# Kernel tuning notes

Hardware: AMD Instinct MI355X
Metric: run time of the kernel (lower is better)

Reference implementation:

```python
import jax, jax.numpy as jnp
import numpy as np

N = 50000   # nodes
E = 800000  # edges (avg degree 16)
D = 96      # feature dim (in = hidden = out)


def setup_inputs() -> dict:
    key = jax.random.key(0)
    ks = jax.random.split(key, 6)
    scale = 1.0 / np.sqrt(D)
    return {
        "x": jax.random.normal(ks[0], (N, D), jnp.float32),
        "edge_index": jax.random.randint(ks[1], (2, E), 0, N, dtype=jnp.int64),
        "W1": jax.random.normal(ks[2], (D, D), jnp.float32) * scale,
        "b1": jnp.zeros((D,), jnp.float32),
        "a1": jnp.full((1,), 0.25, jnp.float32),  # PReLU weight
        "W2": jax.random.normal(ks[3], (D, D), jnp.float32) * scale,
        "b2": jnp.zeros((D,), jnp.float32),
    }


def _gcn_conv(x, W, b, src, dst, norm, n):
    # GCNConv: linear transform, then degree-normalized scatter-add aggregation
    h = x @ W                               # [N, D_out]
    msg = h[src] * norm[:, None]            # gather + scale, [E+N, D_out]
    out = jax.ops.segment_sum(msg, dst, num_segments=n)
    return out + b


def reference(x, edge_index, W1, b1, a1, W2, b2):
    n = x.shape[0]
    # add self loops (PyG gcn_norm default, fill_value=1.0)
    loop = jnp.arange(n, dtype=edge_index.dtype)
    src = jnp.concatenate([edge_index[0], loop])
    dst = jnp.concatenate([edge_index[1], loop])
    # symmetric normalization: D^{-1/2} A D^{-1/2}
    ones = jnp.ones(src.shape[0], dtype=x.dtype)
    deg = jax.ops.segment_sum(ones, dst, num_segments=n)
    dinv = jnp.where(deg > 0, jax.lax.rsqrt(deg), 0.0)
    norm = dinv[src] * dinv[dst]

    h = _gcn_conv(x, W1, b1, src, dst, norm, n)
    h = jnp.where(h > 0, h, a1 * h)  # PReLU (dropout p=0.0 is a no-op)
    h = _gcn_conv(h, W2, b2, src, dst, norm, n)
    return h
```

## Files before the change

### kernel.cpp

```cpp
#include <hip/hip_runtime.h>
#include <hip/hip_bf16.h>

#define NNODES 50000
#define NEDGES 800000
#define DIM    96
#define NBUCK  196
#define CAP    4608
#define TM     64
#define XPAD   104
#define PCH    3125
#define NCHK   256
#define HP     256

typedef __attribute__((ext_vector_type(8))) short   short8;
typedef __attribute__((ext_vector_type(4))) float   float4v;

__device__ __forceinline__ float loadF(const void* p, long i, int isbf) {
    return isbf ? __bfloat162float(((const __hip_bfloat16*)p)[i])
                : ((const float*)p)[i];
}
__device__ __forceinline__ int clampN(int v) {
    return v < 0 ? 0 : (v >= NNODES ? NNODES - 1 : v);
}

__global__ void k_sniff(const unsigned* __restrict__ xw,
                        const unsigned* __restrict__ ew,
                        int* __restrict__ flags) {
    int lane = threadIdx.x;
    int bad = 0, nz = 0;
    for (int r = 0; r < 4; ++r) {
        unsigned w  = xw[lane + 64 * r];
        unsigned lo = w & 0xffffu;
        unsigned ex = (lo >> 7) & 0xffu;
        if (!(lo == 0u || (ex >= 90u && ex <= 145u))) bad++;
        unsigned o = ew[2 * (lane + 64 * r) + 1];
        if (o != 0u) nz++;
    }
    for (int off = 32; off; off >>= 1) {
        bad += __shfl_down(bad, off);
        nz  += __shfl_down(nz,  off);
    }
    if (lane == 0) {
        flags[0] = (bad <= 32) ? 1 : 0;
        flags[1] = (nz  <  4) ? 1 : 0;
    }
}

__global__ __launch_bounds__(256) void k_part(const int* __restrict__ w,
                                              const int* __restrict__ flags,
                                              int* __restrict__ hist,
                                              int* __restrict__ hoff,
                                              unsigned* __restrict__ ebuf) {
    __shared__ unsigned pack[PCH];
    __shared__ unsigned opack[PCH];
    __shared__ int h[256];
    __shared__ int sc[256];
    const int is64 = flags[1];
    const int tid = threadIdx.x;
    const int blk = blockIdx.x;
    const int e0  = blk * PCH;

    h[tid] = 0;
    __syncthreads();
    if (is64) {
        const long long* wl = (const long long*)w;
        for (int k = tid; k < PCH; k += 256) {
            int s = clampN((int)wl[e0 + k]);
            int d = clampN((int)wl[NEDGES + e0 + k]);
            pack[k] = ((unsigned)d << 16) | (unsigned)s;
            atomicAdd(&h[d >> 8], 1);
        }
    } else {
        for (int k = tid; k < PCH; k += 256) {
            int s = clampN(w[e0 + k]);
            int d = clampN(w[NEDGES + e0 + k]);
            pack[k] = ((unsigned)d << 16) | (unsigned)s;
            atomicAdd(&h[d >> 8], 1);
        }
    }
    __syncthreads();
    int v = h[tid];
    sc[tid] = v;
    __syncthreads();
    for (int off = 1; off < 256; off <<= 1) {
        int t2 = (tid >= off) ? sc[tid - off] : 0;
        __syncthreads();
        sc[tid] += t2;
        __syncthreads();
    }
    const int excl = sc[tid] - v;
    hist[blk * HP + tid] = v;
    hoff[blk * HP + tid] = excl;
    h[tid] = excl;
    __syncthreads();
    for (int k = tid; k < PCH; k += 256) {
        unsigned r = pack[k];
        int pos = atomicAdd(&h[(r >> 16) >> 8], 1);
        opack[pos] = r;
    }
    __syncthreads();
    for (int k = tid; k < PCH; k += 256)
        ebuf[e0 + k] = opack[k];
}

__global__ __launch_bounds__(512) void k_csr(const unsigned* __restrict__ ebuf,
                                             const int* __restrict__ hist,
                                             const int* __restrict__ hoff,
                                             int* __restrict__ rowbeg,
                                             int* __restrict__ rowend,
                                             unsigned short* __restrict__ col,
                                             float* __restrict__ dinv) {
    __shared__ int h256[256];
    __shared__ int sc[256];
    __shared__ int cur[256];
    __shared__ int scnt[256];
    __shared__ int soff[256];
    const int b   = blockIdx.x;
    const int tid = threadIdx.x;

    if (tid < 256) {
        scnt[tid] = hist[tid * HP + b];
        soff[tid] = hoff[tid * HP + b];
        h256[tid] = 0;
    }
    __syncthreads();
    const int ch  = tid >> 1;
    const int par = tid & 1;
    {
        const int cnt = scnt[ch];
        const int off = ch * PCH + soff[ch];
        for (int j = par; j < cnt; j += 2)
            atomicAdd(&h256[(ebuf[off + j] >> 16) & 255], 1);
    }
    __syncthreads();
    int v = 0;
    if (tid < 256) { v = h256[tid]; sc[tid] = v; }
    __syncthreads();
    for (int off = 1; off < 256; off <<= 1) {
        int t2 = 0;
        if (tid < 256 && tid >= off) t2 = sc[tid - off];
        __syncthreads();
        if (tid < 256) sc[tid] += t2;
        __syncthreads();
    }
    if (tid < 256) {
        int start = b * CAP + sc[tid] - v;
        cur[tid] = start;
        int node = b * 256 + tid;
        if (node < NNODES) {
            rowbeg[node] = start;
            rowend[node] = start + v;
            dinv[node] = rsqrtf((float)v + 1.0f);
        }
    }
    __syncthreads();
    {
        const int cnt = scnt[ch];
        const int off = ch * PCH + soff[ch];
        const int lim = (b + 1) * CAP;
        for (int j = par; j < cnt; j += 2) {
            unsigned r = ebuf[off + j];
            int pos = atomicAdd(&cur[(r >> 16) & 255], 1);
            if (pos < lim) col[pos] = (unsigned short)(r & 0xffffu);
        }
    }
}

__global__ __launch_bounds__(256) void k_gemm_mfma(
        const void* __restrict__ X, int x_force_bf16,
        const void* __restrict__ W,
        const float* __restrict__ dinv,
        __hip_bfloat16* __restrict__ g,
        const int* __restrict__ flags) {
    __shared__ __hip_bfloat16 Xs[TM * XPAD];
    __shared__ __hip_bfloat16 Wt[DIM * XPAD];

    const int t    = threadIdx.x;
    const int fbf  = flags[0];
    const int xbf  = x_force_bf16 ? 1 : fbf;
    const int row0 = blockIdx.x * TM;

    if (!fbf) {
        const float4* Wv = (const float4*)W;
        for (int idx = t; idx < DIM * DIM / 4; idx += 256) {
            int k = idx / (DIM / 4);
            int n = (idx - k * (DIM / 4)) * 4;
            float4 w4 = Wv[idx];
            Wt[(n + 0) * XPAD + k] = __float2bfloat16(w4.x);
            Wt[(n + 1) * XPAD + k] = __float2bfloat16(w4.y);
            Wt[(n + 2) * XPAD + k] = __float2bfloat16(w4.z);
            Wt[(n + 3) * XPAD + k] = __float2bfloat16(w4.w);
        }
    } else {
        for (int idx = t; idx < DIM * DIM; idx += 256) {
            int k = idx / DIM, n = idx - k * DIM;
            Wt[n * XPAD + k] = __float2bfloat16(loadF(W, idx, 1));
        }
    }
    if (!xbf) {
        const float4* Xv = (const float4*)X;
        for (int idx = t; idx < TM * (DIM / 4); idx += 256) {
            int r = idx / (DIM / 4);
            int c = (idx - r * (DIM / 4)) * 4;
            int gr = row0 + r;
            float4 vv = {0.f, 0.f, 0.f, 0.f};
            if (gr < NNODES) vv = Xv[(size_t)gr * (DIM / 4) + (c >> 2)];
            *(__hip_bfloat162*)&Xs[r * XPAD + c] =
                __halves2bfloat162(__float2bfloat16(vv.x), __float2bfloat16(vv.y));
            *(__hip_bfloat162*)&Xs[r * XPAD + c + 2] =
                __halves2bfloat162(__float2bfloat16(vv.z), __float2bfloat16(vv.w));
        }
    } else {
        const short* Xs16 = (const short*)X;
        for (int idx = t; idx < TM * (DIM / 8); idx += 256) {
            int r  = idx / (DIM / 8);
            int c8 = idx - r * (DIM / 8);
            int gr = row0 + r;
            short8 vv = {0, 0, 0, 0, 0, 0, 0, 0};
            if (gr < NNODES) vv = *(const short8*)(Xs16 + (size_t)gr * DIM + c8 * 8);
            *(short8*)((short*)Xs + r * XPAD + c8 * 8) = vv;
        }
    }
    __syncthreads();

    const int wave = t >> 6;
    const int lane = t & 63;
    const int m    = lane & 15;
    const int quad = lane >> 4;

    const short* xsp = (const short*)Xs;
    short8 a[3];
#pragma unroll
    for (int kt = 0; kt < 3; ++kt)
        a[kt] = *(const short8*)(xsp + (wave * 16 + m) * XPAD + kt * 32 + quad * 8);

    float dv[4];
#pragma unroll
    for (int r2 = 0; r2 < 4; ++r2) {
        int gr = row0 + wave * 16 + quad * 4 + r2;
        dv[r2] = (gr < NNODES) ? dinv[gr] : 0.f;
    }

    const short* wtp = (const short*)Wt;
#pragma unroll
    for (int nt = 0; nt < 6; ++nt) {
        float4v acc = {0.f, 0.f, 0.f, 0.f};
#pragma unroll
        for (int kt = 0; kt < 3; ++kt) {
            short8 b = *(const short8*)(wtp + (nt * 16 + m) * XPAD + kt * 32 + quad * 8);
            acc = __builtin_amdgcn_mfma_f32_16x16x32_bf16(a[kt], b, acc, 0, 0, 0);
        }
#pragma unroll
        for (int r2 = 0; r2 < 4; ++r2) {
            int gr = row0 + wave * 16 + quad * 4 + r2;
            if (gr < NNODES)
                g[(size_t)gr * DIM + nt * 16 + m] = __float2bfloat16(acc[r2] * dv[r2]);
        }
    }
}

__global__ __launch_bounds__(256) void k_aggr(
        const __hip_bfloat16* __restrict__ g,
        const int* __restrict__ rowbeg,
        const int* __restrict__ rowend,
        const unsigned short* __restrict__ col,
        const float* __restrict__ dinv,
        const void* __restrict__ b,
        const void* __restrict__ a1,
        void* __restrict__ out,
        const int* __restrict__ flags, int prelu) {
    const int wave = threadIdx.x >> 6;
    const int lane = threadIdx.x & 63;
    const int row  = blockIdx.x * 4 + wave;
    if (row >= NNODES) return;
    const int fbf = flags[0];
    const __hip_bfloat162* gv = (const __hip_bfloat162*)g;
    const int c = lane;

    float2 acc = {0.f, 0.f};
    if (c < 48) acc = __bfloat1622float2(gv[(size_t)row * 48 + c]);

    const int p0 = rowbeg[row], p1 = rowend[row];
    int i = p0;
    for (; i + 16 <= p1; i += 16) {
        int s[16];
#pragma unroll
        for (int k = 0; k < 16; ++k) s[k] = col[i + k];
        if (c < 48) {
            float2 v[16];
#pragma unroll
            for (int k = 0; k < 16; ++k)
                v[k] = __bfloat1622float2(gv[(size_t)s[k] * 48 + c]);
            float2 t0, t1, t2, t3;
            t0.x = (v[0].x + v[1].x) + (v[2].x + v[3].x);
            t0.y = (v[0].y + v[1].y) + (v[2].y + v[3].y);
            t1.x = (v[4].x + v[5].x) + (v[6].x + v[7].x);
            t1.y = (v[4].y + v[5].y) + (v[6].y + v[7].y);
            t2.x = (v[8].x + v[9].x) + (v[10].x + v[11].x);
            t2.y = (v[8].y + v[9].y) + (v[10].y + v[11].y);
            t3.x = (v[12].x + v[13].x) + (v[14].x + v[15].x);
            t3.y = (v[12].y + v[13].y) + (v[14].y + v[15].y);
            acc.x += (t0.x + t1.x) + (t2.x + t3.x);
            acc.y += (t0.y + t1.y) + (t2.y + t3.y);
        }
    }
    if (i < p1) {
        const int last = p1 - 1;
        int s[16];
#pragma unroll
        for (int k = 0; k < 16; ++k) {
            int idx = i + k;
            s[k] = col[idx > last ? last : idx];
        }
        if (c < 48) {
            float2 v[16];
#pragma unroll
            for (int k = 0; k < 16; ++k) {
                v[k] = __bfloat1622float2(gv[(size_t)s[k] * 48 + c]);
                if (i + k > last) { v[k].x = 0.f; v[k].y = 0.f; }
            }
            float2 t0, t1, t2, t3;
            t0.x = (v[0].x + v[1].x) + (v[2].x + v[3].x);
            t0.y = (v[0].y + v[1].y) + (v[2].y + v[3].y);
            t1.x = (v[4].x + v[5].x) + (v[6].x + v[7].x);
            t1.y = (v[4].y + v[5].y) + (v[6].y + v[7].y);
            t2.x = (v[8].x + v[9].x) + (v[10].x + v[11].x);
            t2.y = (v[8].y + v[9].y) + (v[10].y + v[11].y);
            t3.x = (v[12].x + v[13].x) + (v[14].x + v[15].x);
            t3.y = (v[12].y + v[13].y) + (v[14].y + v[15].y);
            acc.x += (t0.x + t1.x) + (t2.x + t3.x);
            acc.y += (t0.y + t1.y) + (t2.y + t3.y);
        }
    }

    if (c < 48) {
        float dv = dinv[row];
        float vx = dv * acc.x + loadF(b, 2 * c,     fbf);
        float vy = dv * acc.y + loadF(b, 2 * c + 1, fbf);
        if (prelu) {
            float alpha = loadF(a1, 0, fbf);
            vx = vx > 0.f ? vx : alpha * vx;
            vy = vy > 0.f ? vy : alpha * vy;
            ((__hip_bfloat162*)out)[(size_t)row * 48 + c] =
                __halves2bfloat162(__float2bfloat16(vx), __float2bfloat16(vy));
        } else if (fbf) {
            ((__hip_bfloat162*)out)[(size_t)row * 48 + c] =
                __halves2bfloat162(__float2bfloat16(vx), __float2bfloat16(vy));
        } else {
            float2 o; o.x = vx; o.y = vy;
            ((float2*)out)[(size_t)row * 48 + c] = o;
        }
    }
}

extern "C" void kernel_launch(void* const* d_in, const int* in_sizes, int n_in,
                              void* d_out, int out_size, void* d_ws, size_t ws_size,
                              hipStream_t stream) {
    const void* x  = d_in[0];
    const int*  ei = (const int*)d_in[1];
    const void* W1 = d_in[2];
    const void* b1 = d_in[3];
    const void* a1 = d_in[4];
    const void* W2 = d_in[5];
    const void* b2 = d_in[6];

    size_t off = 0;
    auto alloc = [&](size_t bytes) { size_t p = off; off = (off + bytes + 255) & ~(size_t)255; return p; };
    char* ws = (char*)d_ws;
    int*            flags  = (int*)           (ws + alloc(1024));
    float*          dinv   = (float*)         (ws + alloc((size_t)NNODES * 4));
    int*            rowbeg = (int*)           (ws + alloc((size_t)NNODES * 4));
    int*            rowend = (int*)           (ws + alloc((size_t)NNODES * 4));
    int*            hist   = (int*)           (ws + alloc((size_t)NCHK * HP * 4));
    int*            hoff   = (int*)           (ws + alloc((size_t)NCHK * HP * 4));
    unsigned*       ebuf   = (unsigned*)      (ws + alloc((size_t)NEDGES * 4));
    unsigned short* col    = (unsigned short*)(ws + alloc((size_t)NBUCK * CAP * 2 + 256));
    __hip_bfloat16* g      = (__hip_bfloat16*)(ws + alloc((size_t)NNODES * DIM * 2));
    __hip_bfloat16* g2     = (__hip_bfloat16*)(ws + alloc((size_t)NNODES * DIM * 2));
    if (ws_size < off) return;

    k_sniff<<<1, 64, 0, stream>>>((const unsigned*)x, (const unsigned*)ei, flags);
    k_part <<<NCHK, 256, 0, stream>>>(ei, flags, hist, hoff, ebuf);
    k_csr  <<<NBUCK, 512, 0, stream>>>(ebuf, hist, hoff, rowbeg, rowend, col, dinv);

    const int gemm_grid = (NNODES + TM - 1) / TM;
    const int aggr_grid = (NNODES + 3) / 4;

    k_gemm_mfma<<<gemm_grid, 256, 0, stream>>>(x, 0, W1, dinv, g, flags);
    k_aggr<<<aggr_grid, 256, 0, stream>>>(g, rowbeg, rowend, col, dinv, b1, a1, g2, flags, 1);

    k_gemm_mfma<<<gemm_grid, 256, 0, stream>>>(g2, 1, W2, dinv, g, flags);
    k_aggr<<<aggr_grid, 256, 0, stream>>>(g, rowbeg, rowend, col, dinv, b2, a1, d_out, flags, 0);
}
```

Before: 192.3 us.

## Fuse sniff, partition and CSR build into one kernel with a grid barrier

```diff
diff --git a/kernel.cpp b/kernel.cpp
--- a/kernel.cpp
+++ b/kernel.cpp
@@ -15,6 +15,8 @@
 typedef __attribute__((ext_vector_type(8))) short   short8;
 typedef __attribute__((ext_vector_type(4))) float   float4v;
 
+__device__ int g_bar[2] = {0, 0};
+
 __device__ __forceinline__ float loadF(const void* p, long i, int isbf) {
     return isbf ? __bfloat162float(((const __hip_bfloat16*)p)[i])
                 : ((const float*)p)[i];
@@ -23,105 +25,108 @@
     return v < 0 ? 0 : (v >= NNODES ? NNODES - 1 : v);
 }
 
-__global__ void k_sniff(const unsigned* __restrict__ xw,
-                        const unsigned* __restrict__ ew,
-                        int* __restrict__ flags) {
-    int lane = threadIdx.x;
-    int bad = 0, nz = 0;
-    for (int r = 0; r < 4; ++r) {
-        unsigned w  = xw[lane + 64 * r];
-        unsigned lo = w & 0xffffu;
-        unsigned ex = (lo >> 7) & 0xffu;
-        if (!(lo == 0u || (ex >= 90u && ex <= 145u))) bad++;
-        unsigned o = ew[2 * (lane + 64 * r) + 1];
-        if (o != 0u) nz++;
-    }
-    for (int off = 32; off; off >>= 1) {
-        bad += __shfl_down(bad, off);
-        nz  += __shfl_down(nz,  off);
-    }
-    if (lane == 0) {
-        flags[0] = (bad <= 32) ? 1 : 0;
-        flags[1] = (nz  <  4) ? 1 : 0;
-    }
-}
-
-__global__ __launch_bounds__(256) void k_part(const int* __restrict__ w,
-                                              const int* __restrict__ flags,
-                                              int* __restrict__ hist,
-                                              int* __restrict__ hoff,
-                                              unsigned* __restrict__ ebuf) {
+__device__ __forceinline__ void gbar(int slot) {
+    __syncthreads();
+    if (threadIdx.x == 0) {
+        __threadfence();
+        atomicAdd(&g_bar[slot], 1);
+        while (atomicAdd(&g_bar[slot], 0) < NCHK) __builtin_amdgcn_s_sleep(2);
+        __threadfence();
+    }
+    __syncthreads();
+}
+
+__global__ __launch_bounds__(512) void k_build(
+        const unsigned* __restrict__ xw,
+        const int* __restrict__ ew,
+        int* __restrict__ flags,
+        int* __restrict__ hist,
+        int* __restrict__ hoff,
+        unsigned* __restrict__ ebuf,
+        int* __restrict__ rowbeg,
+        int* __restrict__ rowend,
+        unsigned short* __restrict__ col,
+        float* __restrict__ dinv) {
     __shared__ unsigned pack[PCH];
     __shared__ unsigned opack[PCH];
     __shared__ int h[256];
     __shared__ int sc[256];
-    const int is64 = flags[1];
+    __shared__ int cur[256];
+    __shared__ int scnt[256];
+    __shared__ int soff[256];
+    __shared__ int sn[2];
     const int tid = threadIdx.x;
     const int blk = blockIdx.x;
-    const int e0  = blk * PCH;
-
-    h[tid] = 0;
-    __syncthreads();
+
+    if (tid < 2) sn[tid] = 0;
+    __syncthreads();
+    if (tid < 256) {
+        unsigned w  = xw[tid];
+        unsigned lo = w & 0xffffu;
+        unsigned ex = (lo >> 7) & 0xffu;
+        if (!(lo == 0u || (ex >= 90u && ex <= 145u))) atomicAdd(&sn[0], 1);
+        if (((const unsigned*)ew)[2 * tid + 1] != 0u)  atomicAdd(&sn[1], 1);
+    }
+    __syncthreads();
+    const int is64 = (sn[1] < 4) ? 1 : 0;
+    if (blk == 0 && tid == 0) {
+        flags[0] = (sn[0] <= 32) ? 1 : 0;
+        flags[1] = is64;
+    }
+
+    if (tid < 256) h[tid] = 0;
+    __syncthreads();
+    const int e0 = blk * PCH;
     if (is64) {
-        const long long* wl = (const long long*)w;
-        for (int k = tid; k < PCH; k += 256) {
+        const long long* wl = (const long long*)ew;
+        for (int k = tid; k < PCH; k += 512) {
             int s = clampN((int)wl[e0 + k]);
             int d = clampN((int)wl[NEDGES + e0 + k]);
             pack[k] = ((unsigned)d << 16) | (unsigned)s;
             atomicAdd(&h[d >> 8], 1);
         }
     } else {
-        for (int k = tid; k < PCH; k += 256) {
-            int s = clampN(w[e0 + k]);
-            int d = clampN(w[NEDGES + e0 + k]);
+        for (int k = tid; k < PCH; k += 512) {
+            int s = clampN(ew[e0 + k]);
+            int d = clampN(ew[NEDGES + e0 + k]);
             pack[k] = ((unsigned)d << 16) | (unsigned)s;
             atomicAdd(&h[d >> 8], 1);
         }
     }
     __syncthreads();
-    int v = h[tid];
-    sc[tid] = v;
+    int v0 = 0;
+    if (tid < 256) { v0 = h[tid]; sc[tid] = v0; }
     __syncthreads();
     for (int off = 1; off < 256; off <<= 1) {
-        int t2 = (tid >= off) ? sc[tid - off] : 0;
+        int t2 = 0;
+        if (tid < 256 && tid >= off) t2 = sc[tid - off];
         __syncthreads();
-        sc[tid] += t2;
+        if (tid < 256) sc[tid] += t2;
         __syncthreads();
     }
-    const int excl = sc[tid] - v;
-    hist[blk * HP + tid] = v;
-    hoff[blk * HP + tid] = excl;
-    h[tid] = excl;
-    __syncthreads();
-    for (int k = tid; k < PCH; k += 256) {
+    if (tid < 256) {
+        int excl = sc[tid] - v0;
+        hist[blk * HP + tid] = v0;
+        hoff[blk * HP + tid] = excl;
+        h[tid] = excl;
+    }
+    __syncthreads();
+    for (int k = tid; k < PCH; k += 512) {
         unsigned r = pack[k];
         int pos = atomicAdd(&h[(r >> 16) >> 8], 1);
         opack[pos] = r;
     }
     __syncthreads();
-    for (int k = tid; k < PCH; k += 256)
+    for (int k = tid; k < PCH; k += 512)
         ebuf[e0 + k] = opack[k];
-}
-
-__global__ __launch_bounds__(512) void k_csr(const unsigned* __restrict__ ebuf,
-                                             const int* __restrict__ hist,
-                                             const int* __restrict__ hoff,
-                                             int* __restrict__ rowbeg,
-                                             int* __restrict__ rowend,
-                                             unsigned short* __restrict__ col,
-                                             float* __restrict__ dinv) {
-    __shared__ int h256[256];
-    __shared__ int sc[256];
-    __shared__ int cur[256];
-    __shared__ int scnt[256];
-    __shared__ int soff[256];
-    const int b   = blockIdx.x;
-    const int tid = threadIdx.x;
-
+
+    gbar(0);
+
+    if (blk >= NBUCK) return;
     if (tid < 256) {
-        scnt[tid] = hist[tid * HP + b];
-        soff[tid] = hoff[tid * HP + b];
-        h256[tid] = 0;
+        scnt[tid] = hist[tid * HP + blk];
+        soff[tid] = hoff[tid * HP + blk];
+        h[tid] = 0;
     }
     __syncthreads();
     const int ch  = tid >> 1;
@@ -130,11 +135,11 @@
         const int cnt = scnt[ch];
         const int off = ch * PCH + soff[ch];
         for (int j = par; j < cnt; j += 2)
-            atomicAdd(&h256[(ebuf[off + j] >> 16) & 255], 1);
+            atomicAdd(&h[(ebuf[off + j] >> 16) & 255], 1);
     }
     __syncthreads();
     int v = 0;
-    if (tid < 256) { v = h256[tid]; sc[tid] = v; }
+    if (tid < 256) { v = h[tid]; sc[tid] = v; }
     __syncthreads();
     for (int off = 1; off < 256; off <<= 1) {
         int t2 = 0;
@@ -144,9 +149,9 @@
         __syncthreads();
     }
     if (tid < 256) {
-        int start = b * CAP + sc[tid] - v;
+        int start = blk * CAP + sc[tid] - v;
         cur[tid] = start;
-        int node = b * 256 + tid;
+        int node = blk * 256 + tid;
         if (node < NNODES) {
             rowbeg[node] = start;
             rowend[node] = start + v;
@@ -157,7 +162,7 @@
     {
         const int cnt = scnt[ch];
         const int off = ch * PCH + soff[ch];
-        const int lim = (b + 1) * CAP;
+        const int lim = (blk + 1) * CAP;
         for (int j = par; j < cnt; j += 2) {
             unsigned r = ebuf[off + j];
             int pos = atomicAdd(&cur[(r >> 16) & 255], 1);
@@ -175,7 +180,11 @@
     __shared__ __hip_bfloat16 Xs[TM * XPAD];
     __shared__ __hip_bfloat16 Wt[DIM * XPAD];
 
-    const int t    = threadIdx.x;
+    const int t = threadIdx.x;
+    if (blockIdx.x == 0 && t == 0) {
+        atomicExch(&g_bar[0], 0);
+        atomicExch(&g_bar[1], 0);
+    }
     const int fbf  = flags[0];
     const int xbf  = x_force_bf16 ? 1 : fbf;
     const int row0 = blockIdx.x * TM;
@@ -379,9 +388,8 @@
     __hip_bfloat16* g2     = (__hip_bfloat16*)(ws + alloc((size_t)NNODES * DIM * 2));
     if (ws_size < off) return;
 
-    k_sniff<<<1, 64, 0, stream>>>((const unsigned*)x, (const unsigned*)ei, flags);
-    k_part <<<NCHK, 256, 0, stream>>>(ei, flags, hist, hoff, ebuf);
-    k_csr  <<<NBUCK, 512, 0, stream>>>(ebuf, hist, hoff, rowbeg, rowend, col, dinv);
+    k_build<<<NCHK, 512, 0, stream>>>((const unsigned*)x, ei, flags,
+                                      hist, hoff, ebuf, rowbeg, rowend, col, dinv);
 
     const int gemm_grid = (NNODES + TM - 1) / TM;
     const int aggr_grid = (NNODES + 3) / 4;
```

After: 209.7 us. 9.1% more time.

## Split aggregation into column slices with lanes sharing neighbors and shuffle reduction

Applied to the files above, without the earlier changes.

```diff
diff --git a/kernel.cpp b/kernel.cpp
--- a/kernel.cpp
+++ b/kernel.cpp
@@ -269,86 +269,70 @@
         const void* __restrict__ a1,
         void* __restrict__ out,
         const int* __restrict__ flags, int prelu) {
-    const int wave = threadIdx.x >> 6;
-    const int lane = threadIdx.x & 63;
-    const int row  = blockIdx.x * 4 + wave;
-    if (row >= NNODES) return;
-    const int fbf = flags[0];
+    const int wave  = threadIdx.x >> 6;
+    const int lane  = threadIdx.x & 63;
+    const int slice = blockIdx.x & 7;
+    const int rblk  = blockIdx.x >> 3;
+    const int p     = lane >> 3;
+    const int n     = lane & 7;
+    const bool act  = p < 6;
+    const int cp    = slice * 6 + (act ? p : 5);
+    const int fbf   = flags[0];
     const __hip_bfloat162* gv = (const __hip_bfloat162*)g;
-    const int c = lane;
-
-    float2 acc = {0.f, 0.f};
-    if (c < 48) acc = __bfloat1622float2(gv[(size_t)row * 48 + c]);
-
-    const int p0 = rowbeg[row], p1 = rowend[row];
-    int i = p0;
-    for (; i + 16 <= p1; i += 16) {
-        int s[16];
-#pragma unroll
-        for (int k = 0; k < 16; ++k) s[k] = col[i + k];
-        if (c < 48) {
-            float2 v[16];
-#pragma unroll
-            for (int k = 0; k < 16; ++k)
-                v[k] = __bfloat1622float2(gv[(size_t)s[k] * 48 + c]);
-            float2 t0, t1, t2, t3;
-            t0.x = (v[0].x + v[1].x) + (v[2].x + v[3].x);
-            t0.y = (v[0].y + v[1].y) + (v[2].y + v[3].y);
-            t1.x = (v[4].x + v[5].x) + (v[6].x + v[7].x);
-            t1.y = (v[4].y + v[5].y) + (v[6].y + v[7].y);
-            t2.x = (v[8].x + v[9].x) + (v[10].x + v[11].x);
-            t2.y = (v[8].y + v[9].y) + (v[10].y + v[11].y);
-            t3.x = (v[12].x + v[13].x) + (v[14].x + v[15].x);
-            t3.y = (v[12].y + v[13].y) + (v[14].y + v[15].y);
-            acc.x += (t0.x + t1.x) + (t2.x + t3.x);
-            acc.y += (t0.y + t1.y) + (t2.y + t3.y);
-        }
-    }
-    if (i < p1) {
-        const int last = p1 - 1;
-        int s[16];
-#pragma unroll
-        for (int k = 0; k < 16; ++k) {
-            int idx = i + k;
-            s[k] = col[idx > last ? last : idx];
-        }
-        if (c < 48) {
-            float2 v[16];
-#pragma unroll
-            for (int k = 0; k < 16; ++k) {
-                v[k] = __bfloat1622float2(gv[(size_t)s[k] * 48 + c]);
-                if (i + k > last) { v[k].x = 0.f; v[k].y = 0.f; }
+
+    const float bx = loadF(b, 2 * cp,     fbf);
+    const float by = loadF(b, 2 * cp + 1, fbf);
+    const float alpha = prelu ? loadF(a1, 0, fbf) : 0.f;
+
+    for (int r = 0; r < 8; ++r) {
+        const int row = rblk * 32 + wave * 8 + r;
+        if (row >= NNODES) return;
+        float2 acc = {0.f, 0.f};
+        {
+            float2 s2 = __bfloat1622float2(gv[(size_t)row * 48 + cp]);
+            if (n == 0) acc = s2;
+        }
+        const int p0 = rowbeg[row], p1 = rowend[row];
+        int i = p0;
+        for (; i + 16 <= p1; i += 16) {
+            int s0 = col[i + n];
+            int s1 = col[i + 8 + n];
+            float2 v0 = __bfloat1622float2(gv[(size_t)s0 * 48 + cp]);
+            float2 v1 = __bfloat1622float2(gv[(size_t)s1 * 48 + cp]);
+            acc.x += v0.x + v1.x;
+            acc.y += v0.y + v1.y;
+        }
+        if (i < p1) {
+            const int last = p1 - 1;
+            int i0 = i + n,     j0 = i0 > last ? last : i0;
+            int i1 = i + 8 + n, j1 = i1 > last ? last : i1;
+            int s0 = col[j0];
+            int s1 = col[j1];
+            float2 v0 = __bfloat1622float2(gv[(size_t)s0 * 48 + cp]);
+            float2 v1 = __bfloat1622float2(gv[(size_t)s1 * 48 + cp]);
+            if (i0 < p1) { acc.x += v0.x; acc.y += v0.y; }
+            if (i1 < p1) { acc.x += v1.x; acc.y += v1.y; }
+        }
+#pragma unroll
+        for (int off = 1; off < 8; off <<= 1) {
+            acc.x += __shfl_xor(acc.x, off);
+            acc.y += __shfl_xor(acc.y, off);
+        }
+        if (n == 0 && act) {
+            float dv = dinv[row];
+            float vx = dv * acc.x + bx;
+            float vy = dv * acc.y + by;
+            if (prelu) {
+                vx = vx > 0.f ? vx : alpha * vx;
+                vy = vy > 0.f ? vy : alpha * vy;
             }
-            float2 t0, t1, t2, t3;
-            t0.x = (v[0].x + v[1].x) + (v[2].x + v[3].x);
-            t0.y = (v[0].y + v[1].y) + (v[2].y + v[3].y);
-            t1.x = (v[4].x + v[5].x) + (v[6].x + v[7].x);
-            t1.y = (v[4].y + v[5].y) + (v[6].y + v[7].y);
-            t2.x = (v[8].x + v[9].x) + (v[10].x + v[11].x);
-            t2.y = (v[8].y + v[9].y) + (v[10].y + v[11].y);
-            t3.x = (v[12].x + v[13].x) + (v[14].x + v[15].x);
-            t3.y = (v[12].y + v[13].y) + (v[14].y + v[15].y);
-            acc.x += (t0.x + t1.x) + (t2.x + t3.x);
-            acc.y += (t0.y + t1.y) + (t2.y + t3.y);
-        }
-    }
-
-    if (c < 48) {
-        float dv = dinv[row];
-        float vx = dv * acc.x + loadF(b, 2 * c,     fbf);
-        float vy = dv * acc.y + loadF(b, 2 * c + 1, fbf);
-        if (prelu) {
-            float alpha = loadF(a1, 0, fbf);
-            vx = vx > 0.f ? vx : alpha * vx;
-            vy = vy > 0.f ? vy : alpha * vy;
-            ((__hip_bfloat162*)out)[(size_t)row * 48 + c] =
-                __halves2bfloat162(__float2bfloat16(vx), __float2bfloat16(vy));
-        } else if (fbf) {
-            ((__hip_bfloat162*)out)[(size_t)row * 48 + c] =
-                __halves2bfloat162(__float2bfloat16(vx), __float2bfloat16(vy));
-        } else {
-            float2 o; o.x = vx; o.y = vy;
-            ((float2*)out)[(size_t)row * 48 + c] = o;
+            if (prelu || fbf) {
+                ((__hip_bfloat162*)out)[(size_t)row * 48 + cp] =
+                    __halves2bfloat162(__float2bfloat16(vx), __float2bfloat16(vy));
+            } else {
+                float2 o; o.x = vx; o.y = vy;
+                ((float2*)out)[(size_t)row * 48 + cp] = o;
+            }
         }
     }
 }
@@ -384,7 +368,7 @@
     k_csr  <<<NBUCK, 512, 0, stream>>>(ebuf, hist, hoff, rowbeg, rowend, col, dinv);
 
     const int gemm_grid = (NNODES + TM - 1) / TM;
-    const int aggr_grid = (NNODES + 3) / 4;
+    const int aggr_grid = ((NNODES + 31) / 32) * 8;
 
     k_gemm_mfma<<<gemm_grid, 256, 0, stream>>>(x, 0, W1, dinv, g, flags);
     k_aggr<<<aggr_grid, 256, 0, stream>>>(g, rowbeg, rowend, col, dinv, b1, a1, g2, flags, 1);
```

After: 373.0 us. 1.94x slower.
